# Optimization experiments

Measured on AMD Instinct MI355X. Metric: run time of the kernel, lower is better.

## Reference

```python
import jax, jax.numpy as jnp
import numpy as np

N, T, D = 64, 4096, 128


def setup_inputs() -> dict:
    key = jax.random.key(0)
    k1, k2, k3, k4 = jax.random.split(key, 4)
    return {
        "query": jax.random.normal(k1, (N, D), dtype=jnp.float32),
        "key": jax.random.normal(k2, (T, N, D), dtype=jnp.float32),
        "value": jax.random.normal(k3, (T, N, D), dtype=jnp.float32),
        "speech_len": jax.random.randint(k4, (N,), 0, T, dtype=jnp.int64),
    }


def reference(query, key, value, speech_len):
    # energy[n, t] = <key[t, n, :], query[n, :]>   (torch: bmm(key^T, q).squeeze)
    energy = jnp.einsum("tnd,nd->nt", key, query)  # (N, T)
    # per-row length mask: mask[i, :speech_len[i]] = 1
    t_idx = jnp.arange(energy.shape[1])
    mask = (t_idx[None, :] < speech_len[:, None]).astype(energy.dtype)  # (N, T)
    # faithful to source: multiplicative mask (zeros energy, NOT -inf)
    score = jax.nn.softmax(mask * energy, axis=1)
    # redundant renormalization kept for faithfulness
    score = score / jnp.sum(score, axis=1, keepdims=True)
    # context[n, v] = sum_t score[n, t] * value[t, n, v]
    context = jnp.einsum("nt,tnv->nv", score, value)  # (N, D)
    return context, mask
```

## Files before the change

kernel.cpp:

```cpp
#include <hip/hip_runtime.h>

#define N_  64
#define T_  4096
#define D_  128
#define CH_ 32
#define TC_ (T_ / CH_)

__global__ __launch_bounds__(256) void chunk_kernel(
    const float* __restrict__ key, const float* __restrict__ value,
    const float* __restrict__ query, const int* __restrict__ slen,
    float* __restrict__ mask_out, float* __restrict__ m_ws,
    float* __restrict__ s_ws, float* __restrict__ acc_ws)
{
    const int n    = blockIdx.x / CH_;
    const int c    = blockIdx.x % CH_;
    const int tid  = threadIdx.x;
    const int lane = tid & 63;
    const int wv   = tid >> 6;
    const int half = lane >> 5;
    const int hl   = lane & 31;
    const int tbase = c * TC_;
    const int len   = slen[n];

    __shared__ float  ep[TC_];
    __shared__ float  wred[8];
    __shared__ float4 red[4][32];

    const float4 q4 = *reinterpret_cast<const float4*>(query + n * D_ + hl * 4);

    const size_t rowstride2 = (size_t)2 * N_ * D_;
    const float* krow = key   + ((size_t)(tbase + wv * 32 + half) * N_ + n) * D_ + hl * 4;
    const float* vrow = value + ((size_t)(tbase + wv * 32 + half) * N_ + n) * D_ + hl * 4;

    float4 kbuf[16];
    #pragma unroll
    for (int i = 0; i < 16; ++i)
        kbuf[i] = *reinterpret_cast<const float4*>(krow + (size_t)i * rowstride2);

    #pragma unroll
    for (int i = 0; i < 16; ++i) {
        float p = kbuf[i].x * q4.x + kbuf[i].y * q4.y
                + kbuf[i].z * q4.z + kbuf[i].w * q4.w;
        #pragma unroll
        for (int off = 16; off; off >>= 1) p += __shfl_xor(p, off, 64);
        const int lt = wv * 32 + i * 2 + half;
        if (hl == 0) ep[lt] = (tbase + lt < len) ? p : 0.f;
    }

    float4 vbuf[16];
    #pragma unroll
    for (int i = 0; i < 16; ++i)
        vbuf[i] = *reinterpret_cast<const float4*>(vrow + (size_t)i * rowstride2);

    __syncthreads();

    const float ev = (tid < TC_) ? ep[tid] : -3.4e38f;
    float m = ev;
    #pragma unroll
    for (int off = 32; off; off >>= 1) m = fmaxf(m, __shfl_xor(m, off, 64));
    if (lane == 0) wred[wv] = m;
    __syncthreads();
    m = fmaxf(fmaxf(wred[0], wred[1]), fmaxf(wred[2], wred[3]));

    float sp = 0.f;
    if (tid < TC_) {
        const float p = __expf(ev - m);
        ep[tid] = p;
        sp = p;
        mask_out[n * T_ + tbase + tid] = (tbase + tid < len) ? 1.f : 0.f;
    }
    #pragma unroll
    for (int off = 32; off; off >>= 1) sp += __shfl_xor(sp, off, 64);
    if (lane == 0) wred[4 + wv] = sp;
    __syncthreads();
    if (tid == 0) {
        m_ws[n * CH_ + c] = m;
        s_ws[n * CH_ + c] = wred[4] + wred[5] + wred[6] + wred[7];
    }

    float4 acc = make_float4(0.f, 0.f, 0.f, 0.f);
    #pragma unroll
    for (int i = 0; i < 16; ++i) {
        const float pv = ep[wv * 32 + i * 2 + half];
        acc.x += pv * vbuf[i].x; acc.y += pv * vbuf[i].y;
        acc.z += pv * vbuf[i].z; acc.w += pv * vbuf[i].w;
    }
    acc.x += __shfl_xor(acc.x, 32, 64);
    acc.y += __shfl_xor(acc.y, 32, 64);
    acc.z += __shfl_xor(acc.z, 32, 64);
    acc.w += __shfl_xor(acc.w, 32, 64);
    if (half == 0) red[wv][hl] = acc;
    __syncthreads();
    if (tid < 32) {
        const float4 a = red[0][tid], b = red[1][tid];
        const float4 e = red[2][tid], d = red[3][tid];
        float4 r;
        r.x = (a.x + b.x) + (e.x + d.x);
        r.y = (a.y + b.y) + (e.y + d.y);
        r.z = (a.z + b.z) + (e.z + d.z);
        r.w = (a.w + b.w) + (e.w + d.w);
        *reinterpret_cast<float4*>(acc_ws + ((size_t)(n * CH_ + c)) * D_ + tid * 4) = r;
    }
}

__global__ __launch_bounds__(64) void finalize_kernel(
    const float* __restrict__ m_ws, const float* __restrict__ s_ws,
    const float* __restrict__ acc_ws, float* __restrict__ ctx)
{
    const int n    = blockIdx.x;
    const int lane = threadIdx.x;

    const float mc = (lane < CH_) ? m_ws[n * CH_ + lane] : -3.4e38f;
    float M = mc;
    #pragma unroll
    for (int off = 32; off; off >>= 1) M = fmaxf(M, __shfl_xor(M, off, 64));

    const float ew = (lane < CH_) ? __expf(mc - M) : 0.f;
    float S = (lane < CH_) ? s_ws[n * CH_ + lane] * ew : 0.f;
    #pragma unroll
    for (int off = 32; off; off >>= 1) S += __shfl_xor(S, off, 64);

    float2 r = make_float2(0.f, 0.f);
    #pragma unroll 8
    for (int c = 0; c < CH_; ++c) {
        const float w = __shfl(ew, c, 64);
        const float2 a = *reinterpret_cast<const float2*>(
            acc_ws + ((size_t)(n * CH_ + c)) * D_ + lane * 2);
        r.x += w * a.x; r.y += w * a.y;
    }
    const float invS = 1.f / S;
    *reinterpret_cast<float2*>(ctx + n * D_ + lane * 2) =
        make_float2(r.x * invS, r.y * invS);
}

extern "C" void kernel_launch(void* const* d_in, const int* in_sizes, int n_in,
                              void* d_out, int out_size, void* d_ws, size_t ws_size,
                              hipStream_t stream) {
    const float* query = (const float*)d_in[0];
    const float* key   = (const float*)d_in[1];
    const float* value = (const float*)d_in[2];
    const int*   slen  = (const int*)d_in[3];

    float* out      = (float*)d_out;
    float* ctx_out  = out;
    float* mask_out = out + N_ * D_;

    float* m_ws   = (float*)d_ws;
    float* s_ws   = m_ws + N_ * CH_;
    float* acc_ws = s_ws + N_ * CH_;

    chunk_kernel<<<N_ * CH_, 256, 0, stream>>>(key, value, query, slen,
                                               mask_out, m_ws, s_ws, acc_ws);
    finalize_kernel<<<N_, 64, 0, stream>>>(m_ws, s_ws, acc_ws, ctx_out);
}
```

Measured before the change: 279.2 us.

## Restructure split-softmax into contiguous time slabs covering all batch rows

Each block now handles 16 consecutive time steps for all 64 batch rows. The key and value reads therefore cover contiguous 32KB rows of the [T,N,D] tensors, instead of strided per-batch rows. The per-slab softmax is done entirely within a 32-lane half-wave, with no shared memory or block barriers. This makes 256 partials per batch row, so the finalize kernel is widened to 256 threads with a shared-memory reduction. The risks are a much larger workspace and finalize cost, plus a serial loop over 8 batch rows per half-wave that may limit memory-level parallelism.

```diff
diff --git a/kernel.cpp b/kernel.cpp
--- a/kernel.cpp
+++ b/kernel.cpp
@@ -3,134 +3,126 @@
 #define N_  64
 #define T_  4096
 #define D_  128
-#define CH_ 32
-#define TC_ (T_ / CH_)
+#define TS_ 16
+#define SL_ (T_ / TS_)
 
-__global__ __launch_bounds__(256) void chunk_kernel(
+__global__ __launch_bounds__(256) void slab_kernel(
     const float* __restrict__ key, const float* __restrict__ value,
     const float* __restrict__ query, const int* __restrict__ slen,
     float* __restrict__ mask_out, float* __restrict__ m_ws,
     float* __restrict__ s_ws, float* __restrict__ acc_ws)
 {
-    const int n    = blockIdx.x / CH_;
-    const int c    = blockIdx.x % CH_;
+    const int slab = blockIdx.x;
+    const int t0   = slab * TS_;
     const int tid  = threadIdx.x;
-    const int lane = tid & 63;
-    const int wv   = tid >> 6;
-    const int half = lane >> 5;
-    const int hl   = lane & 31;
-    const int tbase = c * TC_;
-    const int len   = slen[n];
+    const int h    = tid >> 5;
+    const int hl   = tid & 31;
 
-    __shared__ float  ep[TC_];
-    __shared__ float  wred[8];
-    __shared__ float4 red[4][32];
+    float4 qb[8];
+    #pragma unroll
+    for (int j = 0; j < 8; ++j)
+        qb[j] = *reinterpret_cast<const float4*>(query + (h * 8 + j) * D_ + hl * 4);
 
-    const float4 q4 = *reinterpret_cast<const float4*>(query + n * D_ + hl * 4);
+    const size_t st = (size_t)N_ * D_;
 
-    const size_t rowstride2 = (size_t)2 * N_ * D_;
-    const float* krow = key   + ((size_t)(tbase + wv * 32 + half) * N_ + n) * D_ + hl * 4;
-    const float* vrow = value + ((size_t)(tbase + wv * 32 + half) * N_ + n) * D_ + hl * 4;
+    for (int j = 0; j < 8; ++j) {
+        const int n   = h * 8 + j;
+        const int len = slen[n];
+        const float4 qj = qb[j];
+        const float* kr = key   + ((size_t)t0 * N_ + n) * D_ + hl * 4;
+        const float* vr = value + ((size_t)t0 * N_ + n) * D_ + hl * 4;
 
-    float4 kbuf[16];
-    #pragma unroll
-    for (int i = 0; i < 16; ++i)
-        kbuf[i] = *reinterpret_cast<const float4*>(krow + (size_t)i * rowstride2);
+        float4 kb[TS_];
+        #pragma unroll
+        for (int t = 0; t < TS_; ++t)
+            kb[t] = *reinterpret_cast<const float4*>(kr + (size_t)t * st);
+        float4 vb[TS_];
+        #pragma unroll
+        for (int t = 0; t < TS_; ++t)
+            vb[t] = *reinterpret_cast<const float4*>(vr + (size_t)t * st);
 
-    #pragma unroll
-    for (int i = 0; i < 16; ++i) {
-        float p = kbuf[i].x * q4.x + kbuf[i].y * q4.y
-                + kbuf[i].z * q4.z + kbuf[i].w * q4.w;
+        float e[TS_];
         #pragma unroll
-        for (int off = 16; off; off >>= 1) p += __shfl_xor(p, off, 64);
-        const int lt = wv * 32 + i * 2 + half;
-        if (hl == 0) ep[lt] = (tbase + lt < len) ? p : 0.f;
-    }
+        for (int t = 0; t < TS_; ++t) {
+            float p = kb[t].x * qj.x + kb[t].y * qj.y
+                    + kb[t].z * qj.z + kb[t].w * qj.w;
+            #pragma unroll
+            for (int off = 16; off; off >>= 1) p += __shfl_xor(p, off, 64);
+            e[t] = (t0 + t < len) ? p : 0.f;
+        }
 
-    float4 vbuf[16];
-    #pragma unroll
-    for (int i = 0; i < 16; ++i)
-        vbuf[i] = *reinterpret_cast<const float4*>(vrow + (size_t)i * rowstride2);
+        float m = e[0];
+        #pragma unroll
+        for (int t = 1; t < TS_; ++t) m = fmaxf(m, e[t]);
+        float s = 0.f;
+        #pragma unroll
+        for (int t = 0; t < TS_; ++t) { e[t] = __expf(e[t] - m); s += e[t]; }
 
-    __syncthreads();
+        float4 a = make_float4(0.f, 0.f, 0.f, 0.f);
+        #pragma unroll
+        for (int t = 0; t < TS_; ++t) {
+            a.x += e[t] * vb[t].x; a.y += e[t] * vb[t].y;
+            a.z += e[t] * vb[t].z; a.w += e[t] * vb[t].w;
+        }
 
-    const float ev = (tid < TC_) ? ep[tid] : -3.4e38f;
-    float m = ev;
-    #pragma unroll
-    for (int off = 32; off; off >>= 1) m = fmaxf(m, __shfl_xor(m, off, 64));
-    if (lane == 0) wred[wv] = m;
-    __syncthreads();
-    m = fmaxf(fmaxf(wred[0], wred[1]), fmaxf(wred[2], wred[3]));
-
-    float sp = 0.f;
-    if (tid < TC_) {
-        const float p = __expf(ev - m);
-        ep[tid] = p;
-        sp = p;
-        mask_out[n * T_ + tbase + tid] = (tbase + tid < len) ? 1.f : 0.f;
-    }
-    #pragma unroll
-    for (int off = 32; off; off >>= 1) sp += __shfl_xor(sp, off, 64);
-    if (lane == 0) wred[4 + wv] = sp;
-    __syncthreads();
-    if (tid == 0) {
-        m_ws[n * CH_ + c] = m;
-        s_ws[n * CH_ + c] = wred[4] + wred[5] + wred[6] + wred[7];
-    }
-
-    float4 acc = make_float4(0.f, 0.f, 0.f, 0.f);
-    #pragma unroll
-    for (int i = 0; i < 16; ++i) {
-        const float pv = ep[wv * 32 + i * 2 + half];
-        acc.x += pv * vbuf[i].x; acc.y += pv * vbuf[i].y;
-        acc.z += pv * vbuf[i].z; acc.w += pv * vbuf[i].w;
-    }
-    acc.x += __shfl_xor(acc.x, 32, 64);
-    acc.y += __shfl_xor(acc.y, 32, 64);
-    acc.z += __shfl_xor(acc.z, 32, 64);
-    acc.w += __shfl_xor(acc.w, 32, 64);
-    if (half == 0) red[wv][hl] = acc;
-    __syncthreads();
-    if (tid < 32) {
-        const float4 a = red[0][tid], b = red[1][tid];
-        const float4 e = red[2][tid], d = red[3][tid];
-        float4 r;
-        r.x = (a.x + b.x) + (e.x + d.x);
-        r.y = (a.y + b.y) + (e.y + d.y);
-        r.z = (a.z + b.z) + (e.z + d.z);
-        r.w = (a.w + b.w) + (e.w + d.w);
-        *reinterpret_cast<float4*>(acc_ws + ((size_t)(n * CH_ + c)) * D_ + tid * 4) = r;
+        if (hl == 0) { m_ws[n * SL_ + slab] = m; s_ws[n * SL_ + slab] = s; }
+        *reinterpret_cast<float4*>(acc_ws + ((size_t)n * SL_ + slab) * D_ + hl * 4) = a;
+        if (hl < TS_)
+            mask_out[n * T_ + t0 + hl] = (t0 + hl < len) ? 1.f : 0.f;
     }
 }
 
-__global__ __launch_bounds__(64) void finalize_kernel(
+__global__ __launch_bounds__(256) void finalize_kernel(
     const float* __restrict__ m_ws, const float* __restrict__ s_ws,
     const float* __restrict__ acc_ws, float* __restrict__ ctx)
 {
     const int n    = blockIdx.x;
-    const int lane = threadIdx.x;
+    const int tid  = threadIdx.x;
+    const int lane = tid & 63;
+    const int wv   = tid >> 6;
 
-    const float mc = (lane < CH_) ? m_ws[n * CH_ + lane] : -3.4e38f;
-    float M = mc;
+    __shared__ float w[SL_];
+    __shared__ float red[8];
+    __shared__ float2 red2[4][64];
+
+    const float mv = m_ws[n * SL_ + tid];
+    float m = mv;
     #pragma unroll
-    for (int off = 32; off; off >>= 1) M = fmaxf(M, __shfl_xor(M, off, 64));
+    for (int off = 32; off; off >>= 1) m = fmaxf(m, __shfl_xor(m, off, 64));
+    if (lane == 0) red[wv] = m;
+    __syncthreads();
+    const float M = fmaxf(fmaxf(red[0], red[1]), fmaxf(red[2], red[3]));
 
-    const float ew = (lane < CH_) ? __expf(mc - M) : 0.f;
-    float S = (lane < CH_) ? s_ws[n * CH_ + lane] * ew : 0.f;
+    const float wgt = __expf(mv - M);
+    w[tid] = wgt;
+    float sv = s_ws[n * SL_ + tid] * wgt;
     #pragma unroll
-    for (int off = 32; off; off >>= 1) S += __shfl_xor(S, off, 64);
+    for (int off = 32; off; off >>= 1) sv += __shfl_xor(sv, off, 64);
+    if (lane == 0) red[4 + wv] = sv;
+    __syncthreads();
+    const float S = red[4] + red[5] + red[6] + red[7];
 
+    const float2* acc2 = reinterpret_cast<const float2*>(acc_ws);
+    const int d2 = tid & 63;
+    const int sg = tid >> 6;
     float2 r = make_float2(0.f, 0.f);
     #pragma unroll 8
-    for (int c = 0; c < CH_; ++c) {
-        const float w = __shfl(ew, c, 64);
-        const float2 a = *reinterpret_cast<const float2*>(
-            acc_ws + ((size_t)(n * CH_ + c)) * D_ + lane * 2);
-        r.x += w * a.x; r.y += w * a.y;
+    for (int s = sg; s < SL_; s += 4) {
+        const float ws_ = w[s];
+        const float2 a = acc2[((size_t)n * SL_ + s) * (D_ / 2) + d2];
+        r.x += ws_ * a.x; r.y += ws_ * a.y;
     }
-    const float invS = 1.f / S;
-    *reinterpret_cast<float2*>(ctx + n * D_ + lane * 2) =
-        make_float2(r.x * invS, r.y * invS);
+    red2[sg][d2] = r;
+    __syncthreads();
+    if (sg == 0) {
+        const float2 a = red2[0][d2], b = red2[1][d2];
+        const float2 c = red2[2][d2], d = red2[3][d2];
+        const float invS = 1.f / S;
+        float2 o;
+        o.x = ((a.x + b.x) + (c.x + d.x)) * invS;
+        o.y = ((a.y + b.y) + (c.y + d.y)) * invS;
+        *reinterpret_cast<float2*>(ctx + n * D_ + d2 * 2) = o;
+    }
 }
 
 extern "C" void kernel_launch(void* const* d_in, const int* in_sizes, int n_in,
@@ -146,10 +138,10 @@
     float* mask_out = out + N_ * D_;
 
     float* m_ws   = (float*)d_ws;
-    float* s_ws   = m_ws + N_ * CH_;
-    float* acc_ws = s_ws + N_ * CH_;
+    float* s_ws   = m_ws + N_ * SL_;
+    float* acc_ws = s_ws + N_ * SL_;
 
-    chunk_kernel<<<N_ * CH_, 256, 0, stream>>>(key, value, query, slen,
-                                               mask_out, m_ws, s_ws, acc_ws);
-    finalize_kernel<<<N_, 64, 0, stream>>>(m_ws, s_ws, acc_ws, ctx_out);
+    slab_kernel<<<SL_, 256, 0, stream>>>(key, value, query, slen,
+                                         mask_out, m_ws, s_ws, acc_ws);
+    finalize_kernel<<<N_, 256, 0, stream>>>(m_ws, s_ws, acc_ws, ctx_out);
 }
```

After: 295.0 us. +5.7%, slower.

## Pair adjacent heads per block and skip key loads past sequence length

Applied to the files above, without the earlier changes.

Each block now covers two adjacent batch rows over 64 timesteps instead of one row over 128. A wave therefore reads a contiguous 1 KB span of key and value per timestep rather than 512 B. Key rows at or beyond speech_len are not loaded at all, because their energy is zeroed by the multiplicative mask anyway, which cuts key traffic roughly in proportion to the masked fraction. Loads now use nontemporal builtins, and the chunk count doubles, so the finalize kernel merges 64 partial softmax chunks per row instead of 32.

```diff
diff --git a/kernel.cpp b/kernel.cpp
--- a/kernel.cpp
+++ b/kernel.cpp
@@ -3,103 +3,105 @@
 #define N_  64
 #define T_  4096
 #define D_  128
-#define CH_ 32
+#define CH_ 64
 #define TC_ (T_ / CH_)
 
-__global__ __launch_bounds__(256) void chunk_kernel(
+typedef float f4v __attribute__((ext_vector_type(4)));
+__device__ __forceinline__ f4v nt_load4(const float* p) {
+    return __builtin_nontemporal_load(reinterpret_cast<const f4v*>(p));
+}
+
+__global__ __launch_bounds__(256) void fused_kernel(
     const float* __restrict__ key, const float* __restrict__ value,
     const float* __restrict__ query, const int* __restrict__ slen,
     float* __restrict__ mask_out, float* __restrict__ m_ws,
     float* __restrict__ s_ws, float* __restrict__ acc_ws)
 {
-    const int n    = blockIdx.x / CH_;
-    const int c    = blockIdx.x % CH_;
-    const int tid  = threadIdx.x;
-    const int lane = tid & 63;
-    const int wv   = tid >> 6;
-    const int half = lane >> 5;
-    const int hl   = lane & 31;
-    const int tbase = c * TC_;
+    const int b     = blockIdx.x;
+    const int npair = b & 31;
+    const int c     = b >> 5;
+    const int tid   = threadIdx.x;
+    const int lane  = tid & 63;
+    const int wv    = tid >> 6;
+    const int nl    = lane >> 5;
+    const int d4    = lane & 31;
+    const int n     = npair * 2 + nl;
     const int len   = slen[n];
+    const int t0    = c * 64 + wv * 16;
 
-    __shared__ float  ep[TC_];
-    __shared__ float  wred[8];
-    __shared__ float4 red[4][32];
+    __shared__ float  ep[2][64];
+    __shared__ float4 red[4][64];
 
-    const float4 q4 = *reinterpret_cast<const float4*>(query + n * D_ + hl * 4);
+    const float4 q4 = *reinterpret_cast<const float4*>(query + n * D_ + d4 * 4);
+    const size_t st = (size_t)N_ * D_;
+    const float* kbase = key   + ((size_t)t0 * N_ + npair * 2) * D_ + lane * 4;
+    const float* vbase = value + ((size_t)t0 * N_ + npair * 2) * D_ + lane * 4;
 
-    const size_t rowstride2 = (size_t)2 * N_ * D_;
-    const float* krow = key   + ((size_t)(tbase + wv * 32 + half) * N_ + n) * D_ + hl * 4;
-    const float* vrow = value + ((size_t)(tbase + wv * 32 + half) * N_ + n) * D_ + hl * 4;
+    f4v kb[16];
+    #pragma unroll
+    for (int i = 0; i < 16; ++i) {
+        const int t = t0 + i;
+        kb[i] = (t < len) ? nt_load4(kbase + (size_t)i * st)
+                          : (f4v){0.f, 0.f, 0.f, 0.f};
+    }
+    #pragma unroll
+    for (int i = 0; i < 16; ++i) {
+        float p = kb[i][0] * q4.x + kb[i][1] * q4.y
+                + kb[i][2] * q4.z + kb[i][3] * q4.w;
+        #pragma unroll
+        for (int off = 16; off; off >>= 1) p += __shfl_xor(p, off, 64);
+        const int t = t0 + i;
+        if (d4 == 0) ep[nl][wv * 16 + i] = (t < len) ? p : 0.f;
+    }
 
-    float4 kbuf[16];
+    f4v vb[16];
     #pragma unroll
     for (int i = 0; i < 16; ++i)
-        kbuf[i] = *reinterpret_cast<const float4*>(krow + (size_t)i * rowstride2);
-
-    #pragma unroll
-    for (int i = 0; i < 16; ++i) {
-        float p = kbuf[i].x * q4.x + kbuf[i].y * q4.y
-                + kbuf[i].z * q4.z + kbuf[i].w * q4.w;
-        #pragma unroll
-        for (int off = 16; off; off >>= 1) p += __shfl_xor(p, off, 64);
-        const int lt = wv * 32 + i * 2 + half;
-        if (hl == 0) ep[lt] = (tbase + lt < len) ? p : 0.f;
-    }
-
-    float4 vbuf[16];
-    #pragma unroll
-    for (int i = 0; i < 16; ++i)
-        vbuf[i] = *reinterpret_cast<const float4*>(vrow + (size_t)i * rowstride2);
+        vb[i] = nt_load4(vbase + (size_t)i * st);
 
     __syncthreads();
 
-    const float ev = (tid < TC_) ? ep[tid] : -3.4e38f;
-    float m = ev;
-    #pragma unroll
-    for (int off = 32; off; off >>= 1) m = fmaxf(m, __shfl_xor(m, off, 64));
-    if (lane == 0) wred[wv] = m;
+    if (wv < 2) {
+        const float e = ep[wv][lane];
+        float m = e;
+        #pragma unroll
+        for (int off = 32; off; off >>= 1) m = fmaxf(m, __shfl_xor(m, off, 64));
+        const float p = __expf(e - m);
+        float s = p;
+        #pragma unroll
+        for (int off = 32; off; off >>= 1) s += __shfl_xor(s, off, 64);
+        ep[wv][lane] = p;
+        if (lane == 0) {
+            m_ws[(npair * 2 + wv) * CH_ + c] = m;
+            s_ws[(npair * 2 + wv) * CH_ + c] = s;
+        }
+    } else {
+        const int nn = npair * 2 + (wv - 2);
+        const int t  = c * 64 + lane;
+        mask_out[(size_t)nn * T_ + t] = (t < slen[nn]) ? 1.f : 0.f;
+    }
     __syncthreads();
-    m = fmaxf(fmaxf(wred[0], wred[1]), fmaxf(wred[2], wred[3]));
-
-    float sp = 0.f;
-    if (tid < TC_) {
-        const float p = __expf(ev - m);
-        ep[tid] = p;
-        sp = p;
-        mask_out[n * T_ + tbase + tid] = (tbase + tid < len) ? 1.f : 0.f;
-    }
-    #pragma unroll
-    for (int off = 32; off; off >>= 1) sp += __shfl_xor(sp, off, 64);
-    if (lane == 0) wred[4 + wv] = sp;
-    __syncthreads();
-    if (tid == 0) {
-        m_ws[n * CH_ + c] = m;
-        s_ws[n * CH_ + c] = wred[4] + wred[5] + wred[6] + wred[7];
-    }
 
     float4 acc = make_float4(0.f, 0.f, 0.f, 0.f);
     #pragma unroll
     for (int i = 0; i < 16; ++i) {
-        const float pv = ep[wv * 32 + i * 2 + half];
-        acc.x += pv * vbuf[i].x; acc.y += pv * vbuf[i].y;
-        acc.z += pv * vbuf[i].z; acc.w += pv * vbuf[i].w;
+        const float pv = ep[nl][wv * 16 + i];
+        acc.x += pv * vb[i][0]; acc.y += pv * vb[i][1];
+        acc.z += pv * vb[i][2]; acc.w += pv * vb[i][3];
     }
-    acc.x += __shfl_xor(acc.x, 32, 64);
-    acc.y += __shfl_xor(acc.y, 32, 64);
-    acc.z += __shfl_xor(acc.z, 32, 64);
-    acc.w += __shfl_xor(acc.w, 32, 64);
-    if (half == 0) red[wv][hl] = acc;
+    red[wv][lane] = acc;
     __syncthreads();
-    if (tid < 32) {
-        const float4 a = red[0][tid], b = red[1][tid];
-        const float4 e = red[2][tid], d = red[3][tid];
+    if (tid < 64) {
+        const float4 a = red[0][tid], bb = red[1][tid];
+        const float4 cc = red[2][tid], dd = red[3][tid];
         float4 r;
-        r.x = (a.x + b.x) + (e.x + d.x);
-        r.y = (a.y + b.y) + (e.y + d.y);
-        r.z = (a.z + b.z) + (e.z + d.z);
-        r.w = (a.w + b.w) + (e.w + d.w);
-        *reinterpret_cast<float4*>(acc_ws + ((size_t)(n * CH_ + c)) * D_ + tid * 4) = r;
+        r.x = (a.x + bb.x) + (cc.x + dd.x);
+        r.y = (a.y + bb.y) + (cc.y + dd.y);
+        r.z = (a.z + bb.z) + (cc.z + dd.z);
+        r.w = (a.w + bb.w) + (cc.w + dd.w);
+        *reinterpret_cast<float4*>(
+            acc_ws + ((size_t)(npair * 2 + (tid >> 5)) * CH_ + c) * D_
+                   + (tid & 31) * 4) = r;
     }
 }
 
@@ -110,26 +112,26 @@
     const int n    = blockIdx.x;
     const int lane = threadIdx.x;
 
-    const float mc = (lane < CH_) ? m_ws[n * CH_ + lane] : -3.4e38f;
+    const float mc = m_ws[n * CH_ + lane];
     float M = mc;
     #pragma unroll
     for (int off = 32; off; off >>= 1) M = fmaxf(M, __shfl_xor(M, off, 64));
 
-    const float ew = (lane < CH_) ? __expf(mc - M) : 0.f;
-    float S = (lane < CH_) ? s_ws[n * CH_ + lane] * ew : 0.f;
+    const float w = __expf(mc - M);
+    float S = s_ws[n * CH_ + lane] * w;
     #pragma unroll
     for (int off = 32; off; off >>= 1) S += __shfl_xor(S, off, 64);
 
+    const float2* acc2 = reinterpret_cast<const float2*>(acc_ws);
     float2 r = make_float2(0.f, 0.f);
     #pragma unroll 8
     for (int c = 0; c < CH_; ++c) {
-        const float w = __shfl(ew, c, 64);
-        const float2 a = *reinterpret_cast<const float2*>(
-            acc_ws + ((size_t)(n * CH_ + c)) * D_ + lane * 2);
-        r.x += w * a.x; r.y += w * a.y;
+        const float wc = __shfl(w, c, 64);
+        const float2 a = acc2[((size_t)n * CH_ + c) * (D_ / 2) + lane];
+        r.x += wc * a.x; r.y += wc * a.y;
     }
     const float invS = 1.f / S;
-    *reinterpret_cast<float2*>(ctx + n * D_ + lane * 2) =
+    *reinterpret_cast<float2*>(ctx + (size_t)n * D_ + lane * 2) =
         make_float2(r.x * invS, r.y * invS);
 }
 
@@ -149,7 +151,7 @@
     float* s_ws   = m_ws + N_ * CH_;
     float* acc_ws = s_ws + N_ * CH_;
 
-    chunk_kernel<<<N_ * CH_, 256, 0, stream>>>(key, value, query, slen,
+    fused_kernel<<<32 * CH_, 256, 0, stream>>>(key, value, query, slen,
                                                mask_out, m_ws, s_ws, acc_ws);
     finalize_kernel<<<N_, 64, 0, stream>>>(m_ws, s_ws, acc_ws, ctx_out);
 }
```

After: 251.3 us. -10.0%, faster.
